# Performance work log

Hardware: AMD Instinct MI355X
Metric: run time of the kernel (lower is better)

Reference implementation:

```python
import jax, jax.numpy as jnp
import numpy as np

B, L = 16, 2048          # batch, raw history length
H, S, M = 512, 8, 512    # hidden_dim, sequence_count, max_seq_len
V = 32000                # shared embed_tokens vocab
TG = 64                  # TIME_GAP_BUCKET_COUNT
LN_EPS = 1e-5


def setup_inputs() -> dict:
    key = jax.random.key(0)
    ks = jax.random.split(key, 16)
    f = lambda k, shp, scale=0.02: jax.random.normal(k, shp, jnp.float32) * scale
    return {
        "history_tokens": jax.random.randint(ks[0], (B, L), 0, V),
        "history_post_tokens": jax.random.randint(ks[1], (B, L), 0, V),
        "history_author_tokens": jax.random.randint(ks[2], (B, L), 0, V),
        "history_action_tokens": jax.random.randint(ks[3], (B, L), 0, V),
        "history_time_gap": jax.random.randint(ks[4], (B, L), 0, TG + 1),
        "history_group_ids": jax.random.randint(ks[5], (B, L), 0, S + 1),
        "history_mask": jax.random.randint(ks[6], (B, L), 0, 2).astype(bool),
        "embed_table": f(ks[7], (V, H)),
        "time_gap_table": f(ks[8], (TG + 1, H)).at[0].set(0.0),   # padding_idx=0
        "seq_id_table": f(ks[9], (S + 1, H)).at[0].set(0.0),      # padding_idx=0
        "pos_table": f(ks[10], (M, H)),
        "ln_gamma": jnp.ones((5 * H,), jnp.float32),
        "ln_beta": jnp.zeros((5 * H,), jnp.float32),
        "w1": f(ks[11], (5 * H, 4 * H)),
        "b1": jnp.zeros((4 * H,), jnp.float32),
        "w2": f(ks[12], (4 * H, H)),
        "b2": jnp.zeros((H,), jnp.float32),
        "empty_tokens": f(ks[13], (S, H)),
    }


def _forward(embed_table, time_gap_table, seq_id_table, pos_table, ln_gamma, ln_beta,
             w1, b1, w2, b2, empty_tokens,
             history_tokens, history_post_tokens, history_author_tokens,
             history_action_tokens, history_time_gap, history_group_ids, history_mask):
    # --- event feature construction: 4 shared-vocab lookups + time-gap embedding ---
    h = embed_table[history_tokens]            # [B,L,H]
    p = embed_table[history_post_tokens]
    a = embed_table[history_author_tokens]
    act = embed_table[history_action_tokens]
    gap_idx = jnp.clip(history_time_gap, 0, TG)
    gap = time_gap_table[gap_idx] * (gap_idx != 0)[..., None]  # padding_idx=0 -> zero vec
    x = jnp.concatenate([h, p, a, act, gap], axis=-1)           # [B,L,5H]

    # --- event_projection: LayerNorm -> Linear -> SiLU -> (Dropout eval) -> Linear ---
    mu = x.mean(-1, keepdims=True)
    var = x.var(-1, keepdims=True)
    xn = (x - mu) * jax.lax.rsqrt(var + LN_EPS) * ln_gamma + ln_beta
    mid = jax.nn.silu(xn @ w1 + b1)                             # [B,L,4H]
    event = mid @ w2 + b2                                       # [B,L,H]

    # --- ragged regroup: for each (b, s) gather masked positions with group id s+1,
    #     keep the LAST M of them, scatter to slots 0..count-1 ---
    gid = history_group_ids                                     # [B,L]
    match = history_mask[:, None, :] & (gid[:, None, :] == jnp.arange(1, S + 1)[None, :, None])  # [B,S,L]
    cum = jnp.cumsum(match.astype(jnp.int32), axis=-1)          # rank+1 within group
    count = cum[..., -1]                                        # [B,S]
    offset = jnp.maximum(count - M, 0)                          # drop all but last M
    slot = cum - 1 - offset[..., None]                          # [B,S,L]
    keep = match & (slot >= 0)
    slot = jnp.where(keep, slot, M)                             # M is out-of-range -> dropped

    b_idx = jnp.arange(B)[:, None, None]
    s_idx = jnp.arange(S)[None, :, None]
    states = jnp.zeros((B, S, M, H), event.dtype)
    states = states.at[b_idx, s_idx, slot].set(event[:, None, :, :], mode="drop")
    smask = jnp.zeros((B, S, M), bool)
    smask = smask.at[b_idx, s_idx, slot].set(True, mode="drop")

    # empty groups get the learned empty token at slot 0
    empty = count == 0                                          # [B,S]
    states = states.at[:, :, 0, :].set(
        jnp.where(empty[..., None], empty_tokens[None], states[:, :, 0, :]))
    smask = smask.at[:, :, 0].set(smask[:, :, 0] | empty)

    # positional + sequence-id embeddings, then zero padded slots
    pos = pos_table[None, None]                                 # [1,1,M,H]
    sid = seq_id_table[1:S + 1][None, :, None, :]               # [1,S,1,H]
    states = (states + pos + sid) * smask[..., None].astype(states.dtype)
    return states, smask


def reference(history_tokens, history_post_tokens, history_author_tokens,
              history_action_tokens, history_time_gap, history_group_ids, history_mask,
              embed_table, time_gap_table, seq_id_table, pos_table, ln_gamma, ln_beta,
              w1, b1, w2, b2, empty_tokens):
    return _forward(embed_table, time_gap_table, seq_id_table, pos_table, ln_gamma, ln_beta,
                    w1, b1, w2, b2, empty_tokens,
                    history_tokens, history_post_tokens, history_author_tokens,
                    history_action_tokens, history_time_gap, history_group_ids, history_mask)
```

## Files before the change

### kernel.cpp

```cpp
#include <hip/hip_runtime.h>
#include <hip/hip_bf16.h>
#include <stdint.h>

#define B_ 16
#define L_ 2048
#define H_ 512
#define S_ 8
#define M_ 512
#define TG_ 64
#define NTOK (B_ * L_)
#define FIVEH (5 * H_)
#define FOURH (4 * H_)

typedef __attribute__((ext_vector_type(4))) float f32x4;
typedef __attribute__((ext_vector_type(8))) short bf16x8;

__device__ __forceinline__ short f2bf(float f) {
  unsigned u = __builtin_bit_cast(unsigned, f);
  unsigned r = (u + 0x7FFFu + ((u >> 16) & 1u)) >> 16;
  return (short)r;
}

__device__ __forceinline__ void gload_lds16(const void* g, void* l) {
  __builtin_amdgcn_global_load_lds(
      (const __attribute__((address_space(1))) unsigned int*)g,
      (__attribute__((address_space(3))) unsigned int*)l, 16, 0, 0);
}

#define BAR __builtin_amdgcn_s_barrier()
#define LGKM0 do { asm volatile("s_waitcnt lgkmcnt(0)" ::: "memory"); \
                   __builtin_amdgcn_sched_barrier(0); } while (0)
#define VMW(n) asm volatile("s_waitcnt vmcnt(" #n ")" ::: "memory")
#define PRIO(p) __builtin_amdgcn_s_setprio(p)


#define STAGE(src, isB, slot, half, kt) do {                                  \
    const short* _s = (src) + (size_t)((half) * 128) * K + (kt);              \
    const int _o = ((isB) ? 65536 : 0) + (slot) * 32768 + (half) * 16384;     \
    gload_lds16(_s + (size_t)sr0 * K + sc0, lds + _o + db0);                  \
    gload_lds16(_s + (size_t)sr1 * K + sc1, lds + _o + db1);                  \
  } while (0)

#define LDA(qr, slot) do { const int _b = (slot) * 32768 + aW + (qr) * 8192;  \
    _Pragma("unroll") for (int fm = 0; fm < 4; ++fm)                          \
    _Pragma("unroll") for (int ks = 0; ks < 2; ++ks)                          \
      a[fm][ks] = *(const bf16x8*)(lds + _b + sA[fm][ks]); } while (0)

#define LDB(dst, qc, slot) do { const int _b = (slot) * 32768 + bW + (qc) * 4096; \
    _Pragma("unroll") for (int fn = 0; fn < 2; ++fn)                          \
    _Pragma("unroll") for (int ks = 0; ks < 2; ++ks)                          \
      dst[fn][ks] = *(const bf16x8*)(lds + _b + sB[fn][ks]); } while (0)

#define MFMA16(qr, qc, bs) do {                                               \
    _Pragma("unroll") for (int fm = 0; fm < 4; ++fm)                          \
    _Pragma("unroll") for (int fn = 0; fn < 2; ++fn)                          \
    _Pragma("unroll") for (int ks = 0; ks < 2; ++ks)                          \
      acc[(qr)*4+fm][(qc)*2+fn] = __builtin_amdgcn_mfma_f32_16x16x32_bf16(    \
          a[fm][ks], bs[fn][ks], acc[(qr)*4+fm][(qc)*2+fn], 0, 0, 0); } while (0)

template<int K>
__device__ __forceinline__ void gemm_core(const short* __restrict__ Ag,
                                          const short* __restrict__ Bg,
                                          char* lds, f32x4 (&acc)[8][4],
                                          int tid) {
  constexpr int NITER = K / 128;
  const int lane = tid & 63;
  const int wave = tid >> 6;
  const int wm = wave >> 2;
  const int wn = wave & 3;
  const int la = lane & 15;
  const int hi = lane >> 4;

  const int x = (la & 7) << 4;
  int sA[4][2], sB[2][2];
#pragma unroll
  for (int fm = 0; fm < 4; ++fm)
#pragma unroll
    for (int ks = 0; ks < 2; ++ks)
      sA[fm][ks] = (((fm * 16 + la) * 128) + (ks * 32 + hi * 8) * 2) ^ x;
#pragma unroll
  for (int fn = 0; fn < 2; ++fn)
#pragma unroll
    for (int ks = 0; ks < 2; ++ks)
      sB[fn][ks] = ((((wn & 1) * 64 + fn * 16 + la) * 128) + (ks * 32 + hi * 8) * 2) ^ x;
  const int aW = wm * 16384;
  const int bW = 65536 + (wn >> 1) * 16384;

  const int db0 = tid * 16, db1 = tid * 16 + 8192;
  const int lb0 = db0 ^ (((db0 >> 7) & 7) << 4);
  const int lb1 = db1 ^ (((db1 >> 7) & 7) << 4);
  const int sr0 = lb0 >> 7, sc0 = (lb0 & 127) >> 1;
  const int sr1 = lb1 >> 7, sc1 = (lb1 & 127) >> 1;

  bf16x8 a[4][2], b0v[2][2], b1v[2][2];

  STAGE(Bg, 1, 0, 0, 0); STAGE(Bg, 1, 0, 1, 0);
  STAGE(Ag, 0, 0, 0, 0); STAGE(Ag, 0, 0, 1, 0);
  STAGE(Bg, 1, 1, 0, 64); STAGE(Bg, 1, 1, 1, 64);
  VMW(0);
  BAR;

  for (int i = 0; i < NITER - 1; ++i) {
    const int kt1 = (2 * i + 1) * 64, kt2 = kt1 + 64, kt3 = kt1 + 128;
    LDA(0, 0); LDB(b0v, 0, 0); STAGE(Ag, 0, 1, 0, kt1);
    BAR; LGKM0; PRIO(1); MFMA16(0, 0, b0v); PRIO(0); BAR;
    LDB(b1v, 1, 0); STAGE(Ag, 0, 1, 1, kt1);
    BAR; LGKM0; PRIO(1); MFMA16(0, 1, b1v); PRIO(0); BAR;
    LDA(1, 0); STAGE(Bg, 1, 0, 0, kt2);
    BAR; LGKM0; PRIO(1); MFMA16(1, 1, b1v); PRIO(0); BAR;
    STAGE(Bg, 1, 0, 1, kt2);
    BAR; LGKM0; PRIO(1); MFMA16(1, 0, b0v); PRIO(0); VMW(4); BAR;
    LDA(0, 1); LDB(b0v, 0, 1); STAGE(Ag, 0, 0, 0, kt2);
    BAR; LGKM0; PRIO(1); MFMA16(0, 0, b0v); PRIO(0); BAR;
    LDB(b1v, 1, 1); STAGE(Ag, 0, 0, 1, kt2);
    BAR; LGKM0; PRIO(1); MFMA16(0, 1, b1v); PRIO(0); BAR;
    LDA(1, 1); STAGE(Bg, 1, 1, 0, kt3);
    BAR; LGKM0; PRIO(1); MFMA16(1, 1, b1v); PRIO(0); BAR;
    STAGE(Bg, 1, 1, 1, kt3);
    BAR; LGKM0; PRIO(1); MFMA16(1, 0, b0v); PRIO(0); VMW(4); BAR;
  }
  {
    const int kt1 = (2 * (NITER - 1) + 1) * 64;
    LDA(0, 0); LDB(b0v, 0, 0); STAGE(Ag, 0, 1, 0, kt1);
    BAR; LGKM0; PRIO(1); MFMA16(0, 0, b0v); PRIO(0); BAR;
    LDB(b1v, 1, 0); STAGE(Ag, 0, 1, 1, kt1);
    BAR; LGKM0; PRIO(1); MFMA16(0, 1, b1v); PRIO(0); BAR;
    LDA(1, 0);
    BAR; LGKM0; PRIO(1); MFMA16(1, 1, b1v); PRIO(0); BAR;
    BAR; LGKM0; PRIO(1); MFMA16(1, 0, b0v); PRIO(0); VMW(0); BAR;
    LDA(0, 1); LDB(b0v, 0, 1);
    BAR; LGKM0; PRIO(1); MFMA16(0, 0, b0v); PRIO(0); BAR;
    LDB(b1v, 1, 1);
    BAR; LGKM0; PRIO(1); MFMA16(0, 1, b1v); PRIO(0); BAR;
    LDA(1, 1);
    BAR; LGKM0; PRIO(1); MFMA16(1, 1, b1v); PRIO(0); BAR;
    BAR; LGKM0; PRIO(1); MFMA16(1, 0, b0v); PRIO(0);
  }
}

__global__ __launch_bounds__(512, 2) void gemm1_kernel(
    const short* __restrict__ A, const short* __restrict__ Bt,
    const float* __restrict__ bias, const int* __restrict__ nkeep,
    short* __restrict__ C) {
  const int nbm = (nkeep[0] + 255) >> 8;
  const int local = blockIdx.x >> 3;
  if (local >= nbm) return;
  const int T = (blockIdx.x & 7) * nbm + local;
  const int bm = T >> 3, bn = T & 7;
  __shared__ __align__(16) char lds[131072];
  const int tid = threadIdx.x;
  f32x4 acc[8][4] = {};
  gemm_core<FIVEH>(A + (size_t)bm * 256 * FIVEH, Bt + (size_t)bn * 256 * FIVEH,
                   lds, acc, tid);
  const int lane = tid & 63, wave = tid >> 6;
  const int wm = wave >> 2, wn = wave & 3;
  const int la = lane & 15, hi = lane >> 4;
  const int row0 = bm * 256 + wm * 128 + hi * 4;
  const int col0 = bn * 256 + wn * 64 + la;
#pragma unroll
  for (int mi = 0; mi < 8; ++mi)
#pragma unroll
    for (int ni = 0; ni < 4; ++ni) {
      const int col = col0 + ni * 16;
      const float bv = bias[col];
#pragma unroll
      for (int r = 0; r < 4; ++r) {
        const int row = row0 + mi * 16 + r;
        float v = acc[mi][ni][r] + bv;
        float sg = 1.f / (1.f + __expf(-v));
        C[(size_t)row * FOURH + col] = f2bf(v * sg);
      }
    }
}

#define ASL(s) ((s) * 32768)
#define BSL(s) (98304 + (s) * 16384)

#define STG2(src, ldsoff, kt) do {                                            \
    const short* _s = (src) + (kt);                                          \
    gload_lds16(_s + (size_t)sr0 * 2048 + sc0, lds + (ldsoff) + db0);         \
    gload_lds16(_s + (size_t)sr1 * 2048 + sc1, lds + (ldsoff) + db1);         \
  } while (0)

#define LDA2(slot) do { const int _b = ASL(slot) + aW2;                       \
    _Pragma("unroll") for (int fm = 0; fm < 4; ++fm)                          \
    _Pragma("unroll") for (int ks = 0; ks < 2; ++ks)                          \
      a[fm][ks] = *(const bf16x8*)(lds + _b + sA2[fm][ks]); } while (0)

#define LDB2a(slot) do { const int _b = BSL(slot);                            \
    _Pragma("unroll") for (int fn = 0; fn < 2; ++fn)                          \
    _Pragma("unroll") for (int ks = 0; ks < 2; ++ks)                          \
      b[fn][ks] = *(const bf16x8*)(lds + _b + sB2[fn][ks]); } while (0)

#define LDB2b(slot) do { const int _b = BSL(slot);                            \
    _Pragma("unroll") for (int fn = 2; fn < 4; ++fn)                          \
    _Pragma("unroll") for (int ks = 0; ks < 2; ++ks)                          \
      b[fn][ks] = *(const bf16x8*)(lds + _b + sB2[fn][ks]); } while (0)

#define MFMA2(h) do {                                                         \
    _Pragma("unroll") for (int fm = 0; fm < 4; ++fm)                          \
    _Pragma("unroll") for (int fn = 2*(h); fn < 2*(h)+2; ++fn)                \
    _Pragma("unroll") for (int ks = 0; ks < 2; ++ks)                          \
      acc[fm][fn] = __builtin_amdgcn_mfma_f32_16x16x32_bf16(                  \
          a[fm][ks], b[fn][ks], acc[fm][fn], 0, 0, 0); } while (0)

#define T2(slot, kt, ISSUE, WAITC) do {                                       \
    LDA2(slot); LDB2a(slot);                                                  \
    if (ISSUE) STG2(Ag, ASL(((slot) + 2) % 3), kt);                           \
    BAR; LGKM0; PRIO(1); MFMA2(0); PRIO(0); BAR;                              \
    LDB2b(slot);                                                              \
    if (ISSUE) { STG2(Ag + 128 * 2048, ASL(((slot) + 2) % 3) + 16384, kt);    \
                 STG2(Bg, BSL(((slot) + 2) % 3), kt); }                       \
    BAR; LGKM0; PRIO(1); MFMA2(1); PRIO(0); WAITC; BAR;                       \
  } while (0)

__global__ __launch_bounds__(512) void gemm2_kernel(
    const short* __restrict__ A, const short* __restrict__ Bt,
    const float* __restrict__ b2, const float* __restrict__ pos,
    const float* __restrict__ sidtab, const int* __restrict__ destv,
    const int* __restrict__ nkeep, float* __restrict__ states) {
  const int bn = blockIdx.x & 3;
  const int bm = blockIdx.x >> 2;
  const int nk = nkeep[0];
  if (bm * 256 >= nk) return;
  __shared__ __align__(16) char lds[147456];
  const int tid = threadIdx.x;
  const int lane = tid & 63, wave = tid >> 6;
  const int wm = wave >> 1;
  const int wn = wave & 1;
  const int la = lane & 15, hi = lane >> 4;
  const short* Ag = A + (size_t)bm * 256 * 2048;
  const short* Bg = Bt + (size_t)bn * 128 * 2048;

  const int x = (la & 7) << 4;
  int sA2[4][2], sB2[4][2];
#pragma unroll
  for (int fm = 0; fm < 4; ++fm)
#pragma unroll
    for (int ks = 0; ks < 2; ++ks)
      sA2[fm][ks] = ((((wm & 1) * 64 + fm * 16 + la) * 128) + (ks * 32 + hi * 8) * 2) ^ x;
#pragma unroll
  for (int fn = 0; fn < 4; ++fn)
#pragma unroll
    for (int ks = 0; ks < 2; ++ks)
      sB2[fn][ks] = (((wn * 64 + fn * 16 + la) * 128) + (ks * 32 + hi * 8) * 2) ^ x;
  const int aW2 = (wm >> 1) * 16384;

  const int db0 = tid * 16, db1 = tid * 16 + 8192;
  const int lb0 = db0 ^ (((db0 >> 7) & 7) << 4);
  const int lb1 = db1 ^ (((db1 >> 7) & 7) << 4);
  const int sr0 = lb0 >> 7, sc0 = (lb0 & 127) >> 1;
  const int sr1 = lb1 >> 7, sc1 = (lb1 & 127) >> 1;

  f32x4 acc[4][4] = {};
  bf16x8 a[4][2], b[4][2];

  STG2(Ag, ASL(0), 0); STG2(Ag + 128 * 2048, ASL(0) + 16384, 0); STG2(Bg, BSL(0), 0);
  STG2(Ag, ASL(1), 64); STG2(Ag + 128 * 2048, ASL(1) + 16384, 64); STG2(Bg, BSL(1), 64);
  VMW(6);
  BAR;
  for (int i = 0; i < 10; ++i) {
    const int kt = i * 192 + 128;
    T2(0, kt, true, VMW(6));
    T2(1, kt + 64, true, VMW(6));
    T2(2, kt + 128, true, VMW(6));
  }
  T2(0, 0, false, VMW(0));
  T2(1, 0, false, ((void)0));

  const int row0 = bm * 256 + wm * 64 + hi * 4;
  const int col0 = bn * 128 + wn * 64 + la;
#pragma unroll
  for (int mi = 0; mi < 4; ++mi) {
#pragma unroll
    for (int r = 0; r < 4; ++r) {
      const int row = row0 + mi * 16 + r;
      if (row >= nk) continue;
      const int dest = destv[row];
      const int slot = dest & (M_ - 1);
      const int gs = dest >> 9;
      const int s = gs & (S_ - 1);
      float* orow = states + (size_t)dest * H_;
#pragma unroll
      for (int n = 0; n < 4; ++n) {
        const int col = col0 + n * 16;
        orow[col] = acc[mi][n][r] + b2[col] + pos[slot * H_ + col] +
                    sidtab[(s + 1) * H_ + col];
      }
    }
  }
}

__global__ __launch_bounds__(256) void transpose_cvt_kernel(
    const float* __restrict__ w1, short* __restrict__ w1T,
    const float* __restrict__ w2, short* __restrict__ w2T) {
  const float* in;
  short* out;
  int K, N;
  if (blockIdx.z == 0) { in = w1; out = w1T; K = FIVEH; N = FOURH; }
  else                 { in = w2; out = w2T; K = FOURH; N = H_; }
  const int n0 = blockIdx.x * 32, k0 = blockIdx.y * 32;
  if (n0 >= N || k0 >= K) return;
  __shared__ float tile[32][33];
  const int tx = threadIdx.x, ty = threadIdx.y;
#pragma unroll
  for (int i = 0; i < 32; i += 8)
    tile[ty + i][tx] = in[(size_t)(k0 + ty + i) * N + n0 + tx];
  __syncthreads();
#pragma unroll
  for (int i = 0; i < 32; i += 8)
    out[(size_t)(n0 + ty + i) * K + k0 + tx] = f2bf(tile[tx][ty + i]);
}

__global__ __launch_bounds__(256) void scan_kernel(
    const int* __restrict__ gid, const int* __restrict__ mask,
    int* __restrict__ counts, int* __restrict__ tokidx,
    int* __restrict__ destv, int* __restrict__ nkeep) {
  const int b = blockIdx.x >> 3;
  const int s = blockIdx.x & 7;
  const int g = s + 1;
  const int base = b * L_;
  const int t = threadIdx.x;
  int loc = 0, sum = 0;
  const int l0 = t * 8;
#pragma unroll
  for (int j = 0; j < 8; ++j) {
    int l = l0 + j;
    bool mt = (mask[base + l] != 0) && (gid[base + l] == g);
    loc |= (mt ? 1 : 0) << j;
    sum += mt ? 1 : 0;
  }
  __shared__ int lds[256];
  __shared__ int basep, offs;
  lds[t] = sum;
  __syncthreads();
  for (int off = 1; off < 256; off <<= 1) {
    int vv = (t >= off) ? lds[t - off] : 0;
    __syncthreads();
    lds[t] += vv;
    __syncthreads();
  }
  if (t == 255) {
    const int cnt = lds[255];
    counts[blockIdx.x] = cnt;
    const int kc = cnt < M_ ? cnt : M_;
    offs = cnt - kc;
    basep = atomicAdd(nkeep, kc);
  }
  __syncthreads();
  int run = lds[t] - sum;
  const int gsM = blockIdx.x * M_;
#pragma unroll
  for (int j = 0; j < 8; ++j) {
    if ((loc >> j) & 1) {
      run += 1;
      const int slot = run - 1 - offs;
      if (slot >= 0) {
        tokidx[basep + slot] = base + l0 + j;
        destv[basep + slot] = gsM + slot;
      }
    }
  }
}

__global__ __launch_bounds__(256) void gather_ln_kernel(
    const int* __restrict__ tokidx, const int* __restrict__ nkeep,
    const int* __restrict__ tok0, const int* __restrict__ tok1,
    const int* __restrict__ tok2, const int* __restrict__ tok3,
    const int* __restrict__ tgap,
    const float* __restrict__ emb, const float* __restrict__ gaptab,
    const float* __restrict__ gamma, const float* __restrict__ beta,
    short* __restrict__ xn) {
  const int wid = threadIdx.x >> 6;
  const int l = threadIdx.x & 63;
  const int j = blockIdx.x * 4 + wid;
  const int nk = nkeep[0];
  const int padded = (nk + 255) & ~255;
  if (j >= padded) return;
  short* orow = xn + (size_t)j * FIVEH;
  if (j >= nk) {
    short4 z = make_short4(0, 0, 0, 0);
#pragma unroll
    for (int i = 0; i < 10; ++i) ((short4*)orow)[i * 64 + l] = z;
    return;
  }
  const int token = tokidx[j];
  const int tk0 = tok0[token], tk1 = tok1[token], tk2 = tok2[token],
            tk3 = tok3[token];
  int gi = tgap[token];
  gi = gi < 0 ? 0 : (gi > TG_ ? TG_ : gi);
  const float4* sb[5];
  sb[0] = (const float4*)(emb + (size_t)tk0 * H_);
  sb[1] = (const float4*)(emb + (size_t)tk1 * H_);
  sb[2] = (const float4*)(emb + (size_t)tk2 * H_);
  sb[3] = (const float4*)(emb + (size_t)tk3 * H_);
  sb[4] = (const float4*)(gaptab + (size_t)gi * H_);
  float4 v[10];
  float sum = 0.f, sq = 0.f;
#pragma unroll
  for (int i = 0; i < 10; ++i) {
    const int d4 = i * 64 + l;
    const int seg = i >> 1;
    float4 xv;
    if (seg < 4 || gi != 0) xv = sb[seg][d4 & 127];
    else xv = make_float4(0.f, 0.f, 0.f, 0.f);
    v[i] = xv;
    sum += xv.x + xv.y + xv.z + xv.w;
    sq += xv.x * xv.x + xv.y * xv.y + xv.z * xv.z + xv.w * xv.w;
  }
#pragma unroll
  for (int s = 32; s; s >>= 1) {
    sum += __shfl_xor(sum, s, 64);
    sq += __shfl_xor(sq, s, 64);
  }
  const float mu = sum * (1.f / FIVEH);
  const float var = sq * (1.f / FIVEH) - mu * mu;
  const float rs = rsqrtf(var + 1e-5f);
#pragma unroll
  for (int i = 0; i < 10; ++i) {
    const int d4 = i * 64 + l;
    const float4 g4 = ((const float4*)gamma)[d4];
    const float4 b4 = ((const float4*)beta)[d4];
    short4 o;
    o.x = f2bf((v[i].x - mu) * rs * g4.x + b4.x);
    o.y = f2bf((v[i].y - mu) * rs * g4.y + b4.y);
    o.z = f2bf((v[i].z - mu) * rs * g4.z + b4.z);
    o.w = f2bf((v[i].w - mu) * rs * g4.w + b4.w);
    ((short4*)orow)[d4] = o;
  }
}

__global__ __launch_bounds__(256) void finalize_kernel(
    const int* __restrict__ counts, const float* __restrict__ empty_tok,
    const float* __restrict__ pos, const float* __restrict__ sidtab,
    float* __restrict__ states, float* __restrict__ smask) {
  const int total = B_ * S_ * M_ * (H_ / 4);
  for (int idx = blockIdx.x * 256 + threadIdx.x; idx < total;
       idx += gridDim.x * 256) {
    const int row = idx >> 7, c = idx & 127;
    const int gs = row >> 9, m = row & (M_ - 1), s = gs & (S_ - 1);
    const int cnt = counts[gs];
    const bool empty = (cnt == 0);
    const bool filled = m < (cnt < M_ ? cnt : M_);
    if (c == 0) smask[row] = (filled || (empty && m == 0)) ? 1.0f : 0.0f;
    if (filled) continue;
    float4 o = make_float4(0.f, 0.f, 0.f, 0.f);
    if (empty && m == 0) {
      float4 e = ((const float4*)(empty_tok + s * H_))[c];
      float4 pv = ((const float4*)pos)[c];
      float4 sd = ((const float4*)(sidtab + (s + 1) * H_))[c];
      o.x = e.x + pv.x + sd.x;
      o.y = e.y + pv.y + sd.y;
      o.z = e.z + pv.z + sd.z;
      o.w = e.w + pv.w + sd.w;
    }
    ((float4*)(states + (size_t)row * H_))[c] = o;
  }
}

extern "C" void kernel_launch(void* const* d_in, const int* in_sizes, int n_in,
                              void* d_out, int out_size, void* d_ws, size_t ws_size,
                              hipStream_t stream) {
  const int* tok0 = (const int*)d_in[0];
  const int* tok1 = (const int*)d_in[1];
  const int* tok2 = (const int*)d_in[2];
  const int* tok3 = (const int*)d_in[3];
  const int* tgap = (const int*)d_in[4];
  const int* gid = (const int*)d_in[5];
  const int* mask = (const int*)d_in[6];
  const float* emb = (const float*)d_in[7];
  const float* gaptab = (const float*)d_in[8];
  const float* sidtab = (const float*)d_in[9];
  const float* pos = (const float*)d_in[10];
  const float* gamma = (const float*)d_in[11];
  const float* beta = (const float*)d_in[12];
  const float* w1 = (const float*)d_in[13];
  const float* b1 = (const float*)d_in[14];
  const float* w2 = (const float*)d_in[15];
  const float* b2 = (const float*)d_in[16];
  const float* empty_tok = (const float*)d_in[17];

  char* p = (char*)d_ws;
  short* xn = (short*)p;  p += (size_t)NTOK * FIVEH * 2;
  short* mid = (short*)p; p += (size_t)NTOK * FOURH * 2;
  short* w1T = (short*)p; p += (size_t)FOURH * FIVEH * 2;
  short* w2T = (short*)p; p += (size_t)H_ * FOURH * 2;
  int* tokidx = (int*)p;  p += (size_t)NTOK * 4;
  int* destv = (int*)p;   p += (size_t)NTOK * 4;
  int* counts = (int*)p;  p += 512;
  int* nkeep = (int*)p;   p += 512;

  float* states = (float*)d_out;
  float* smask = states + (size_t)B_ * S_ * M_ * H_;

  hipMemsetAsync(nkeep, 0, 4, stream);
  transpose_cvt_kernel<<<dim3(FOURH / 32, FIVEH / 32, 2), dim3(32, 8), 0, stream>>>(
      w1, w1T, w2, w2T);
  scan_kernel<<<B_ * S_, 256, 0, stream>>>(gid, mask, counts, tokidx, destv,
                                           nkeep);
  gather_ln_kernel<<<NTOK / 4, 256, 0, stream>>>(tokidx, nkeep, tok0, tok1, tok2,
                                                 tok3, tgap, emb, gaptab, gamma,
                                                 beta, xn);
  gemm1_kernel<<<128 * 8, 512, 0, stream>>>(xn, w1T, b1, nkeep, mid);
  gemm2_kernel<<<128 * 4, 512, 0, stream>>>(mid, w2T, b2, pos, sidtab, destv,
                                            nkeep, states);
  finalize_kernel<<<2048, 256, 0, stream>>>(counts, empty_tok, pos, sidtab,
                                            states, smask);
}
```

Baseline: 264.6 us.

## Merge weight transpose with scan, fold finalize into GEMM2, balance tiles

```diff
diff --git a/kernel.cpp b/kernel.cpp
--- a/kernel.cpp
+++ b/kernel.cpp
@@ -214,15 +214,46 @@
     BAR; LGKM0; PRIO(1); MFMA2(1); PRIO(0); WAITC; BAR;                       \
   } while (0)
 
-__global__ __launch_bounds__(512) void gemm2_kernel(
+__global__ __launch_bounds__(512) void gemm2fin_kernel(
     const short* __restrict__ A, const short* __restrict__ Bt,
     const float* __restrict__ b2, const float* __restrict__ pos,
     const float* __restrict__ sidtab, const int* __restrict__ destv,
-    const int* __restrict__ nkeep, float* __restrict__ states) {
-  const int bn = blockIdx.x & 3;
-  const int bm = blockIdx.x >> 2;
+    const int* __restrict__ nkeep, const int* __restrict__ counts,
+    const float* __restrict__ empty_tok, float* __restrict__ states,
+    float* __restrict__ smask) {
+  if (blockIdx.x >= 512) {
+    const int total = B_ * S_ * M_ * (H_ / 4);
+    for (int idx = (blockIdx.x - 512) * 512 + threadIdx.x; idx < total;
+         idx += 512 * 512) {
+      const int row = idx >> 7, c = idx & 127;
+      const int gs = row >> 9, m = row & (M_ - 1), s = gs & (S_ - 1);
+      const int cnt = counts[gs];
+      const bool empty = (cnt == 0);
+      const bool filled = m < (cnt < M_ ? cnt : M_);
+      if (c == 0) smask[row] = (filled || (empty && m == 0)) ? 1.0f : 0.0f;
+      if (filled) continue;
+      float4 o = make_float4(0.f, 0.f, 0.f, 0.f);
+      if (empty && m == 0) {
+        float4 e = ((const float4*)(empty_tok + s * H_))[c];
+        float4 pv = ((const float4*)pos)[c];
+        float4 sd = ((const float4*)(sidtab + (s + 1) * H_))[c];
+        o.x = e.x + pv.x + sd.x;
+        o.y = e.y + pv.y + sd.y;
+        o.z = e.z + pv.z + sd.z;
+        o.w = e.w + pv.w + sd.w;
+      }
+      ((float4*)(states + (size_t)row * H_))[c] = o;
+    }
+    return;
+  }
   const int nk = nkeep[0];
-  if (bm * 256 >= nk) return;
+  const int ntile = ((nk + 255) >> 8) << 2;
+  const int q = ntile >> 3, r = ntile & 7;
+  const int xg = blockIdx.x & 7, idx = blockIdx.x >> 3;
+  const int cntx = q + (xg < r ? 1 : 0);
+  if (idx >= cntx) return;
+  const int T = xg * q + (xg < r ? xg : r) + idx;
+  const int bm = T >> 2, bn = T & 3;
   __shared__ __align__(16) char lds[147456];
   const int tid = threadIdx.x;
   const int lane = tid & 63, wave = tid >> 6;
@@ -273,8 +304,8 @@
 #pragma unroll
   for (int mi = 0; mi < 4; ++mi) {
 #pragma unroll
-    for (int r = 0; r < 4; ++r) {
-      const int row = row0 + mi * 16 + r;
+    for (int r2 = 0; r2 < 4; ++r2) {
+      const int row = row0 + mi * 16 + r2;
       if (row >= nk) continue;
       const int dest = destv[row];
       const int slot = dest & (M_ - 1);
@@ -284,40 +315,42 @@
 #pragma unroll
       for (int n = 0; n < 4; ++n) {
         const int col = col0 + n * 16;
-        orow[col] = acc[mi][n][r] + b2[col] + pos[slot * H_ + col] +
+        orow[col] = acc[mi][n][r2] + b2[col] + pos[slot * H_ + col] +
                     sidtab[(s + 1) * H_ + col];
       }
     }
   }
 }
 
-__global__ __launch_bounds__(256) void transpose_cvt_kernel(
+__global__ __launch_bounds__(256) void prep_kernel(
     const float* __restrict__ w1, short* __restrict__ w1T,
-    const float* __restrict__ w2, short* __restrict__ w2T) {
-  const float* in;
-  short* out;
-  int K, N;
-  if (blockIdx.z == 0) { in = w1; out = w1T; K = FIVEH; N = FOURH; }
-  else                 { in = w2; out = w2T; K = FOURH; N = H_; }
-  const int n0 = blockIdx.x * 32, k0 = blockIdx.y * 32;
-  if (n0 >= N || k0 >= K) return;
-  __shared__ float tile[32][33];
-  const int tx = threadIdx.x, ty = threadIdx.y;
-#pragma unroll
-  for (int i = 0; i < 32; i += 8)
-    tile[ty + i][tx] = in[(size_t)(k0 + ty + i) * N + n0 + tx];
-  __syncthreads();
-#pragma unroll
-  for (int i = 0; i < 32; i += 8)
-    out[(size_t)(n0 + ty + i) * K + k0 + tx] = f2bf(tile[tx][ty + i]);
-}
-
-__global__ __launch_bounds__(256) void scan_kernel(
+    const float* __restrict__ w2, short* __restrict__ w2T,
     const int* __restrict__ gid, const int* __restrict__ mask,
     int* __restrict__ counts, int* __restrict__ tokidx,
     int* __restrict__ destv, int* __restrict__ nkeep) {
-  const int b = blockIdx.x >> 3;
-  const int s = blockIdx.x & 7;
+  const int bid = blockIdx.x;
+  if (bid < 6144) {
+    const float* in;
+    short* out;
+    int K, N, tt;
+    if (bid < 5120) { in = w1; out = w1T; K = FIVEH; N = FOURH; tt = bid; }
+    else            { in = w2; out = w2T; K = FOURH; N = H_;   tt = bid - 5120; }
+    const int nT = N >> 5;
+    const int n0 = (tt % nT) * 32, k0 = (tt / nT) * 32;
+    __shared__ float tile[32][33];
+    const int tx = threadIdx.x & 31, ty = threadIdx.x >> 5;
+#pragma unroll
+    for (int i = 0; i < 32; i += 8)
+      tile[ty + i][tx] = in[(size_t)(k0 + ty + i) * N + n0 + tx];
+    __syncthreads();
+#pragma unroll
+    for (int i = 0; i < 32; i += 8)
+      out[(size_t)(n0 + ty + i) * K + k0 + tx] = f2bf(tile[tx][ty + i]);
+    return;
+  }
+  const int grp = bid - 6144;
+  const int b = grp >> 3;
+  const int s = grp & 7;
   const int g = s + 1;
   const int base = b * L_;
   const int t = threadIdx.x;
@@ -330,26 +363,26 @@
     loc |= (mt ? 1 : 0) << j;
     sum += mt ? 1 : 0;
   }
-  __shared__ int lds[256];
+  __shared__ int sdata[256];
   __shared__ int basep, offs;
-  lds[t] = sum;
+  sdata[t] = sum;
   __syncthreads();
   for (int off = 1; off < 256; off <<= 1) {
-    int vv = (t >= off) ? lds[t - off] : 0;
+    int vv = (t >= off) ? sdata[t - off] : 0;
     __syncthreads();
-    lds[t] += vv;
+    sdata[t] += vv;
     __syncthreads();
   }
   if (t == 255) {
-    const int cnt = lds[255];
-    counts[blockIdx.x] = cnt;
+    const int cnt = sdata[255];
+    counts[grp] = cnt;
     const int kc = cnt < M_ ? cnt : M_;
     offs = cnt - kc;
     basep = atomicAdd(nkeep, kc);
   }
   __syncthreads();
-  int run = lds[t] - sum;
-  const int gsM = blockIdx.x * M_;
+  int run = sdata[t] - sum;
+  const int gsM = grp * M_;
 #pragma unroll
   for (int j = 0; j < 8; ++j) {
     if ((loc >> j) & 1) {
@@ -427,34 +460,6 @@
     o.z = f2bf((v[i].z - mu) * rs * g4.z + b4.z);
     o.w = f2bf((v[i].w - mu) * rs * g4.w + b4.w);
     ((short4*)orow)[d4] = o;
-  }
-}
-
-__global__ __launch_bounds__(256) void finalize_kernel(
-    const int* __restrict__ counts, const float* __restrict__ empty_tok,
-    const float* __restrict__ pos, const float* __restrict__ sidtab,
-    float* __restrict__ states, float* __restrict__ smask) {
-  const int total = B_ * S_ * M_ * (H_ / 4);
-  for (int idx = blockIdx.x * 256 + threadIdx.x; idx < total;
-       idx += gridDim.x * 256) {
-    const int row = idx >> 7, c = idx & 127;
-    const int gs = row >> 9, m = row & (M_ - 1), s = gs & (S_ - 1);
-    const int cnt = counts[gs];
-    const bool empty = (cnt == 0);
-    const bool filled = m < (cnt < M_ ? cnt : M_);
-    if (c == 0) smask[row] = (filled || (empty && m == 0)) ? 1.0f : 0.0f;
-    if (filled) continue;
-    float4 o = make_float4(0.f, 0.f, 0.f, 0.f);
-    if (empty && m == 0) {
-      float4 e = ((const float4*)(empty_tok + s * H_))[c];
-      float4 pv = ((const float4*)pos)[c];
-      float4 sd = ((const float4*)(sidtab + (s + 1) * H_))[c];
-      o.x = e.x + pv.x + sd.x;
-      o.y = e.y + pv.y + sd.y;
-      o.z = e.z + pv.z + sd.z;
-      o.w = e.w + pv.w + sd.w;
-    }
-    ((float4*)(states + (size_t)row * H_))[c] = o;
   }
 }
 
@@ -494,16 +499,13 @@
   float* smask = states + (size_t)B_ * S_ * M_ * H_;
 
   hipMemsetAsync(nkeep, 0, 4, stream);
-  transpose_cvt_kernel<<<dim3(FOURH / 32, FIVEH / 32, 2), dim3(32, 8), 0, stream>>>(
-      w1, w1T, w2, w2T);
-  scan_kernel<<<B_ * S_, 256, 0, stream>>>(gid, mask, counts, tokidx, destv,
-                                           nkeep);
+  prep_kernel<<<6272, 256, 0, stream>>>(w1, w1T, w2, w2T, gid, mask, counts,
+                                        tokidx, destv, nkeep);
   gather_ln_kernel<<<NTOK / 4, 256, 0, stream>>>(tokidx, nkeep, tok0, tok1, tok2,
                                                  tok3, tgap, emb, gaptab, gamma,
                                                  beta, xn);
   gemm1_kernel<<<128 * 8, 512, 0, stream>>>(xn, w1T, b1, nkeep, mid);
-  gemm2_kernel<<<128 * 4, 512, 0, stream>>>(mid, w2T, b2, pos, sidtab, destv,
-                                            nkeep, states);
-  finalize_kernel<<<2048, 256, 0, stream>>>(counts, empty_tok, pos, sidtab,
-                                            states, smask);
-}
+  gemm2fin_kernel<<<512 + 512, 512, 0, stream>>>(mid, w2T, b2, pos, sidtab,
+                                                 destv, nkeep, counts, empty_tok,
+                                                 states, smask);
+}
```

Measured after the change: 259.9 us. About the same (-1.8%).
